# Kernel optimization log

Hardware: AMD Instinct MI355X
Metric: run time of the kernel (lower is better)

The kernel has to match this reference:

```python
import jax, jax.numpy as jnp
import numpy as np

K = 3
STRIDE = 1
PAD = 1


def _conv2d(x, w, b):
    y = jax.lax.conv_general_dilated(
        x, w, window_strides=(STRIDE, STRIDE),
        padding=[(PAD, PAD), (PAD, PAD)],
        dimension_numbers=("NCHW", "OIHW", "NCHW"))
    return y + b[None, :, None, None]


def _bilinear_sample(xb, py, px):
    # xb: [C, H, W]; py, px: [K2, Ho, Wo] float sample coords
    C, H, W = xb.shape
    y0 = jnp.floor(py)
    x0 = jnp.floor(px)
    ay = py - y0  # frac weights
    ax = px - x0
    out = jnp.zeros((C,) + py.shape, dtype=xb.dtype)
    corners = [
        (y0, x0, (1.0 - ay) * (1.0 - ax)),
        (y0, x0 + 1.0, (1.0 - ay) * ax),
        (y0 + 1.0, x0, ay * (1.0 - ax)),
        (y0 + 1.0, x0 + 1.0, ay * ax),
    ]
    for yc, xc, wgt in corners:
        valid = (yc >= 0) & (yc < H) & (xc >= 0) & (xc < W)
        yi = jnp.clip(yc, 0, H - 1).astype(jnp.int32)
        xi = jnp.clip(xc, 0, W - 1).astype(jnp.int32)
        g = xb[:, yi, xi]  # [C, K2, Ho, Wo]
        out = out + g * (wgt * valid.astype(xb.dtype))[None]
    return out


def _deform_forward(x, weight, bias, p_weight, p_bias):
    B, Cin, H, W = x.shape
    Cout = weight.shape[0]
    K2 = K * K
    # offset / mask prediction conv
    pout = _conv2d(x, p_weight, p_bias)  # [B, 3*K2, Ho, Wo]
    o1, o2, m = jnp.split(pout, 3, axis=1)
    offset = jnp.concatenate([o1, o2], axis=1)  # [B, 2*K2, Ho, Wo]
    mask = jax.nn.sigmoid(m)  # [B, K2, Ho, Wo]
    Ho, Wo = mask.shape[2], mask.shape[3]
    # torchvision layout: channel 2k = dy_k, 2k+1 = dx_k
    off = offset.reshape(B, K2, 2, Ho, Wo)
    dy, dx = off[:, :, 0], off[:, :, 1]  # [B, K2, Ho, Wo]
    ki = (jnp.arange(K2) // K).astype(x.dtype)  # kernel row
    kj = (jnp.arange(K2) % K).astype(x.dtype)   # kernel col
    base_y = jnp.arange(Ho, dtype=x.dtype) * STRIDE - PAD  # [Ho]
    base_x = jnp.arange(Wo, dtype=x.dtype) * STRIDE - PAD  # [Wo]
    py = base_y[None, None, :, None] + ki[None, :, None, None] + dy
    px = base_x[None, None, None, :] + kj[None, :, None, None] + dx
    sampled = jax.vmap(_bilinear_sample)(x, py, px)  # [B, Cin, K2, Ho, Wo]
    sampled = sampled * mask[:, None]
    w = weight.reshape(Cout, Cin, K2)
    out = jnp.einsum('bckhw,ock->bohw', sampled, w) + bias[None, :, None, None]
    return out


def setup_inputs() -> dict:
    key = jax.random.key(0)
    k1, k2, k3 = jax.random.split(key, 3)
    B, Cin, Cout, H, W = 4, 256, 256, 64, 64
    x = jax.random.normal(k1, (B, Cin, H, W), dtype=jnp.float32)
    fan_in = Cin * K * K
    weight = jax.random.normal(k2, (Cout, Cin, K, K), dtype=jnp.float32) / np.sqrt(fan_in)
    bias = jnp.zeros((Cout,), dtype=jnp.float32)
    # small random offset/mask predictor (zero-init in the original; randomized
    # here so the deformable sampling path is exercised)
    p_weight = jax.random.normal(k3, (3 * K * K, Cin, K, K), dtype=jnp.float32) * 0.02
    p_bias = jnp.zeros((3 * K * K,), dtype=jnp.float32)
    return {"x": x, "weight": weight, "bias": bias, "p_weight": p_weight, "p_bias": p_bias}


def reference(x, weight, bias, p_weight, p_bias):
    return _deform_forward(x, weight, bias, p_weight, p_bias)
```

## Files before the change

### kernel.cpp

```cpp
#include <hip/hip_runtime.h>
#include <stdint.h>


#define CIN 256
#define COUT 256
#define HWS 4096
#define MTOT 16384
#define KTOT 2304
#define SPLITK 8

typedef __attribute__((ext_vector_type(8))) short bf16x8;
typedef __attribute__((ext_vector_type(4))) float f32x4;

__device__ __forceinline__ unsigned short f2bf(float f) {
  unsigned int u = __float_as_uint(f);
  unsigned int r = (u + 0x7fffu + ((u >> 16) & 1u)) >> 16;
  return (unsigned short)r;
}
__device__ __forceinline__ float bf2f(unsigned short u) {
  return __uint_as_float(((unsigned int)u) << 16);
}

__device__ __forceinline__ void gload_lds16(const void* g, void* l) {
  __builtin_amdgcn_global_load_lds((const __attribute__((address_space(1))) void*)g,
                                   (__attribute__((address_space(3))) void*)l, 16, 0, 0);
}

__global__ __launch_bounds__(256) void prep_and_transpose(const float* __restrict__ x,
                                                          const float* __restrict__ w,
                                                          const float* __restrict__ pw,
                                                          unsigned short* __restrict__ xt,
                                                          unsigned short* __restrict__ WB,
                                                          unsigned short* __restrict__ PWs,
                                                          unsigned short* __restrict__ zerop) {
  __shared__ float tile[32][33];
  int bid = blockIdx.x;
  if (bid < 4096) {
    int b = bid >> 10;
    int rest = bid & 1023;
    int hw0 = (rest & 127) * 32;
    int c0 = ((rest >> 7) & 7) * 32;
    int tx = threadIdx.x & 31, ty = threadIdx.x >> 5;
    for (int i = ty; i < 32; i += 8)
      tile[i][tx] = x[(size_t)(b * CIN + c0 + i) * HWS + hw0 + tx];
    __syncthreads();
    for (int r = ty; r < 32; r += 8)
      xt[(size_t)(b * HWS + hw0 + r) * CIN + c0 + tx] = f2bf(tile[tx][r]);
  } else {
    int idx = (bid - 4096) * 256 + threadIdx.x;
    if (idx < 512)
      *(uint4*)(zerop + idx * 8) = make_uint4(0, 0, 0, 0);
    if (idx < KTOT * COUT) {
      int f = idx;
      int e = f & 7;
      int row = (f >> 3) & 15;
      int quad = (f >> 7) & 3;
      int j = (f >> 9) & 15;
      int t = f >> 13;
      int kk = t * 32 + quad * 8 + e;
      int o = j * 16 + row;
      int k = kk >> 8, c = kk & 255;
      WB[f] = f2bf(w[o * KTOT + c * 9 + k]);
    } else {
      int f2 = idx - KTOT * COUT;
      int t_ = f2 & 7;
      int rest = f2 >> 3;
      int j = rest & 31;
      int kk = (rest >> 5) * 8 + t_;
      int k = kk >> 8, c = kk & 255;
      float v = (j < 27) ? pw[j * KTOT + c * 9 + k] : 0.0f;
      PWs[f2] = f2bf(v);
    }
  }
}

__global__ __launch_bounds__(256) void offset_conv_sk(const unsigned short* __restrict__ xt,
                                                      const unsigned short* __restrict__ PWs,
                                                      const unsigned short* __restrict__ zerop,
                                                      float* __restrict__ Pbuf) {
  __shared__ unsigned short Al[64 * 32];
  __shared__ unsigned short Bl[1024];
  int tid = threadIdx.x;
  int lane = tid & 63, wv = tid >> 6;
  int mt = (blockIdx.x & 7) * 32 + (blockIdx.x >> 3);
  int m0 = mt * 64;
  int s = blockIdx.y;
  int b = m0 >> 12;
  int hw0 = m0 & 4095;
  f32x4 acc[2] = {};

  for (int tt = 0; tt < 72 / SPLITK; ++tt) {
    int t = s * (72 / SPLITK) + tt;
    int k = t >> 3, c0 = (t & 7) * 32;
    int dyk = k / 3 - 1;
    int dxk = k % 3 - 1;
    __syncthreads();
    if (tid < 128)
      gload_lds16(PWs + (size_t)t * 1024 + tid * 8, &Bl[tid * 8]);
    {
      int r = tid >> 2;
      int hw = hw0 + r;
      int h = hw >> 6, wwp = hw & 63;
      int y = h + dyk, xx = wwp + dxk;
      bool valid = ((unsigned)y < 64u) && ((unsigned)xx < 64u);
      const unsigned short* src = valid
          ? xt + ((size_t)((b << 12) + (y << 6) + xx) << 8) + c0 + (tid & 3) * 8
          : zerop;
      gload_lds16(src, &Al[tid * 8]);
    }
    __syncthreads();
    int row = lane & 15, quad = lane >> 4;
    bf16x8 af = *(const bf16x8*)&Al[(wv * 16 + row) * 32 + quad * 8];
    for (int j = 0; j < 2; ++j) {
      bf16x8 bfr = *(const bf16x8*)&Bl[(quad * 32 + j * 16 + row) * 8];
      acc[j] = __builtin_amdgcn_mfma_f32_16x16x32_bf16(af, bfr, acc[j], 0, 0, 0);
    }
  }

  int row = lane & 15, quad = lane >> 4;
  for (int j = 0; j < 2; ++j) {
    int n = j * 16 + row;
    for (int r_ = 0; r_ < 4; ++r_) {
      int m = m0 + wv * 16 + quad * 4 + r_;
      Pbuf[((size_t)s * MTOT + m) * 32 + n] = acc[j][r_];
    }
  }
}

__global__ __launch_bounds__(256) void sample9(const unsigned short* __restrict__ xt,
                                               const float* __restrict__ Pbuf,
                                               const float* __restrict__ p_bias,
                                               unsigned short* __restrict__ A) {
  __shared__ int4 dI[4][9];
  __shared__ float4 dW[4][9];
  int tid = threadIdx.x;
  int reg = blockIdx.x & 7;
  int mb = reg * 2048 + (blockIdx.x >> 3) * 4;

  if (tid < 36) {
    int lm = tid / 9, k = tid - lm * 9;
    int m = mb + lm;
    float dy = p_bias[2 * k];
    float dx = p_bias[2 * k + 1];
    float mv = p_bias[18 + k];
#pragma unroll
    for (int s = 0; s < SPLITK; ++s) {
      const float* p = Pbuf + ((size_t)s * MTOT + m) * 32;
      dy += p[2 * k];
      dx += p[2 * k + 1];
      mv += p[18 + k];
    }
    float mk = 1.0f / (1.0f + __expf(-mv));

    int hw = m & 4095, h = hw >> 6, ww = hw & 63;
    float py = (float)(h - 1 + k / 3) + dy;
    float px = (float)(ww - 1 + k % 3) + dx;
    float y0f = floorf(py), x0f = floorf(px);
    float ay = py - y0f, ax = px - x0f;
    int y0 = (int)y0f, x0 = (int)x0f;

    float w00 = (1.f - ay) * (1.f - ax) * mk;
    float w01 = (1.f - ay) * ax * mk;
    float w10 = ay * (1.f - ax) * mk;
    float w11 = ay * ax * mk;

    float vy0 = ((unsigned)y0 < 64u) ? 1.f : 0.f;
    float vy1 = ((unsigned)(y0 + 1) < 64u) ? 1.f : 0.f;
    float vx0 = ((unsigned)x0 < 64u) ? 1.f : 0.f;
    float vx1 = ((unsigned)(x0 + 1) < 64u) ? 1.f : 0.f;
    w00 *= vy0 * vx0; w01 *= vy0 * vx1; w10 *= vy1 * vx0; w11 *= vy1 * vx1;

    int yc0 = min(max(y0, 0), 63), yc1 = min(max(y0 + 1, 0), 63);
    int xc0 = min(max(x0, 0), 63), xc1 = min(max(x0 + 1, 0), 63);

    dI[lm][k] = make_int4((yc0 * 64 + xc0) * 256, (yc0 * 64 + xc1) * 256,
                          (yc1 * 64 + xc0) * 256, (yc1 * 64 + xc1) * 256);
    dW[lm][k] = make_float4(w00, w01, w10, w11);
  }
  __syncthreads();

  int wv = tid >> 6, lane = tid & 63;
  int m = mb + wv;
  int b = m >> 12;
  const unsigned short* xtb = xt + (((size_t)b << 12) << 8);
  unsigned short* abase = A + (((size_t)(m >> 4) * 72 + (lane >> 3)) * 16 + (m & 15)) * 32
                            + ((lane >> 1) & 3) * 8 + (lane & 1) * 4;

#pragma unroll
  for (int k = 0; k < 9; ++k) {
    int4 o4 = dI[wv][k];
    float4 w4 = dW[wv][k];
    ushort4 t00 = *(const ushort4*)(xtb + o4.x + 4 * lane);
    ushort4 t01 = *(const ushort4*)(xtb + o4.y + 4 * lane);
    ushort4 t10 = *(const ushort4*)(xtb + o4.z + 4 * lane);
    ushort4 t11 = *(const ushort4*)(xtb + o4.w + 4 * lane);
    float r0 = w4.x * bf2f(t00.x) + w4.y * bf2f(t01.x) + w4.z * bf2f(t10.x) + w4.w * bf2f(t11.x);
    float r1 = w4.x * bf2f(t00.y) + w4.y * bf2f(t01.y) + w4.z * bf2f(t10.y) + w4.w * bf2f(t11.y);
    float r2 = w4.x * bf2f(t00.z) + w4.y * bf2f(t01.z) + w4.z * bf2f(t10.z) + w4.w * bf2f(t11.z);
    float r3 = w4.x * bf2f(t00.w) + w4.y * bf2f(t01.w) + w4.z * bf2f(t10.w) + w4.w * bf2f(t11.w);
    ushort4 o;
    o.x = f2bf(r0); o.y = f2bf(r1); o.z = f2bf(r2); o.w = f2bf(r3);
    *(ushort4*)(abase + (size_t)k * 8 * 512) = o;
  }
}

__global__ __launch_bounds__(256) void main_gemm(const unsigned short* __restrict__ A2,
                                                 const unsigned short* __restrict__ WB,
                                                 const float* __restrict__ bias,
                                                 float* __restrict__ out) {
  int tid = threadIdx.x;
  int lane = tid & 63, wv = tid >> 6;
  int m0 = blockIdx.x * 128;
  int n0 = blockIdx.y * 64;
  int wm = wv * 32;
  int row = lane & 15, quad = lane >> 4;
  f32x4 acc[2][4] = {};

  int mb0 = (m0 + wm) >> 4;
  const unsigned short* aptr0 = A2 + (size_t)mb0 * 72 * 512 + row * 32 + quad * 8;
  const unsigned short* aptr1 = aptr0 + (size_t)72 * 512;
  const unsigned short* bptr = WB + (size_t)(blockIdx.y * 4) * 512 + quad * 128 + row * 8;

  bf16x8 a0c = *(const bf16x8*)(aptr0);
  bf16x8 a1c = *(const bf16x8*)(aptr1);
  bf16x8 bc0 = *(const bf16x8*)(bptr);
  bf16x8 bc1 = *(const bf16x8*)(bptr + 512);
  bf16x8 bc2 = *(const bf16x8*)(bptr + 1024);
  bf16x8 bc3 = *(const bf16x8*)(bptr + 1536);

  for (int t = 0; t < 72; ++t) {
    bf16x8 a0n, a1n, bn0, bn1, bn2, bn3;
    if (t < 71) {
      a0n = *(const bf16x8*)(aptr0 + (t + 1) * 512);
      a1n = *(const bf16x8*)(aptr1 + (t + 1) * 512);
      const unsigned short* bt = bptr + (size_t)(t + 1) * 8192;
      bn0 = *(const bf16x8*)(bt);
      bn1 = *(const bf16x8*)(bt + 512);
      bn2 = *(const bf16x8*)(bt + 1024);
      bn3 = *(const bf16x8*)(bt + 1536);
    }
    acc[0][0] = __builtin_amdgcn_mfma_f32_16x16x32_bf16(a0c, bc0, acc[0][0], 0, 0, 0);
    acc[0][1] = __builtin_amdgcn_mfma_f32_16x16x32_bf16(a0c, bc1, acc[0][1], 0, 0, 0);
    acc[0][2] = __builtin_amdgcn_mfma_f32_16x16x32_bf16(a0c, bc2, acc[0][2], 0, 0, 0);
    acc[0][3] = __builtin_amdgcn_mfma_f32_16x16x32_bf16(a0c, bc3, acc[0][3], 0, 0, 0);
    acc[1][0] = __builtin_amdgcn_mfma_f32_16x16x32_bf16(a1c, bc0, acc[1][0], 0, 0, 0);
    acc[1][1] = __builtin_amdgcn_mfma_f32_16x16x32_bf16(a1c, bc1, acc[1][1], 0, 0, 0);
    acc[1][2] = __builtin_amdgcn_mfma_f32_16x16x32_bf16(a1c, bc2, acc[1][2], 0, 0, 0);
    acc[1][3] = __builtin_amdgcn_mfma_f32_16x16x32_bf16(a1c, bc3, acc[1][3], 0, 0, 0);
    a0c = a0n; a1c = a1n;
    bc0 = bn0; bc1 = bn1; bc2 = bn2; bc3 = bn3;
  }

  int b = m0 >> 12, hw0 = m0 & 4095;
#pragma unroll
  for (int j = 0; j < 4; ++j) {
    int o = n0 + j * 16 + row;
    float bo = bias[o];
#pragma unroll
    for (int i = 0; i < 2; ++i) {
      int hw = hw0 + wm + i * 16 + quad * 4;
      float4 v;
      v.x = acc[i][j][0] + bo;
      v.y = acc[i][j][1] + bo;
      v.z = acc[i][j][2] + bo;
      v.w = acc[i][j][3] + bo;
      *(float4*)(out + (((size_t)(b * COUT + o)) << 12) + hw) = v;
    }
  }
}

extern "C" void kernel_launch(void* const* d_in, const int* in_sizes, int n_in,
                              void* d_out, int out_size, void* d_ws, size_t ws_size,
                              hipStream_t stream) {
  const float* x        = (const float*)d_in[0];
  const float* weight   = (const float*)d_in[1];
  const float* bias     = (const float*)d_in[2];
  const float* p_weight = (const float*)d_in[3];
  const float* p_bias   = (const float*)d_in[4];
  float* out = (float*)d_out;
  char* ws = (char*)d_ws;

  const size_t OFF_XT   = 0;
  const size_t OFF_WB   = OFF_XT + 8388608;
  const size_t OFF_PW   = OFF_WB + 1179648;
  const size_t OFF_P    = OFF_PW + 147456;
  const size_t OFF_ZP   = OFF_P + 16777216;
  const size_t OFF_A    = OFF_ZP + 8192;

  unsigned short* xt    = (unsigned short*)(ws + OFF_XT);
  unsigned short* WB    = (unsigned short*)(ws + OFF_WB);
  unsigned short* PWs   = (unsigned short*)(ws + OFF_PW);
  float* Pbuf           = (float*)(ws + OFF_P);
  unsigned short* zerop = (unsigned short*)(ws + OFF_ZP);
  unsigned short* Amat  = (unsigned short*)(ws + OFF_A);

  prep_and_transpose<<<4096 + 2592, 256, 0, stream>>>(x, weight, p_weight, xt, WB, PWs, zerop);
  offset_conv_sk<<<dim3(MTOT / 64, SPLITK), 256, 0, stream>>>(xt, PWs, zerop, Pbuf);
  sample9<<<MTOT / 4, 256, 0, stream>>>(xt, Pbuf, p_bias, Amat);
  main_gemm<<<dim3(MTOT / 128, COUT / 64), 256, 0, stream>>>(Amat, WB, bias, out);
}
```

Before: 150.3 us.

## Deepen main GEMM register prefetch to four stages and remap blocks per XCD

The main GEMM loop previously prefetched only one k-step ahead. It now keeps four register-staged sets of A/B fragments in flight, so global-load latency is better hidden behind MFMAs. The grid is flattened to 512 blocks and remapped so that the blocks on each XCD share A rows across the four N tiles, which should improve L2 reuse. The extra in-flight fragments raise VGPR pressure and could reduce occupancy.

```diff
diff --git a/kernel.cpp b/kernel.cpp
--- a/kernel.cpp
+++ b/kernel.cpp
@@ -204,52 +204,76 @@
   }
 }
 
+#define LOADSET(SA0, SA1, SB0, SB1, SB2, SB3, TT)                         \
+  {                                                                       \
+    const unsigned short* a0_ = ap0 + (size_t)(TT) * 512;                 \
+    const unsigned short* a1_ = ap1 + (size_t)(TT) * 512;                 \
+    const unsigned short* bt_ = bp + (size_t)(TT) * 8192;                 \
+    SA0 = *(const bf16x8*)(a0_);                                          \
+    SA1 = *(const bf16x8*)(a1_);                                          \
+    SB0 = *(const bf16x8*)(bt_);                                          \
+    SB1 = *(const bf16x8*)(bt_ + 512);                                    \
+    SB2 = *(const bf16x8*)(bt_ + 1024);                                   \
+    SB3 = *(const bf16x8*)(bt_ + 1536);                                   \
+  }
+
+#define COMPUTESET(SA0, SA1, SB0, SB1, SB2, SB3)                                        \
+  acc[0][0] = __builtin_amdgcn_mfma_f32_16x16x32_bf16(SA0, SB0, acc[0][0], 0, 0, 0);    \
+  acc[0][1] = __builtin_amdgcn_mfma_f32_16x16x32_bf16(SA0, SB1, acc[0][1], 0, 0, 0);    \
+  acc[0][2] = __builtin_amdgcn_mfma_f32_16x16x32_bf16(SA0, SB2, acc[0][2], 0, 0, 0);    \
+  acc[0][3] = __builtin_amdgcn_mfma_f32_16x16x32_bf16(SA0, SB3, acc[0][3], 0, 0, 0);    \
+  acc[1][0] = __builtin_amdgcn_mfma_f32_16x16x32_bf16(SA1, SB0, acc[1][0], 0, 0, 0);    \
+  acc[1][1] = __builtin_amdgcn_mfma_f32_16x16x32_bf16(SA1, SB1, acc[1][1], 0, 0, 0);    \
+  acc[1][2] = __builtin_amdgcn_mfma_f32_16x16x32_bf16(SA1, SB2, acc[1][2], 0, 0, 0);    \
+  acc[1][3] = __builtin_amdgcn_mfma_f32_16x16x32_bf16(SA1, SB3, acc[1][3], 0, 0, 0);
+
 __global__ __launch_bounds__(256) void main_gemm(const unsigned short* __restrict__ A2,
                                                  const unsigned short* __restrict__ WB,
                                                  const float* __restrict__ bias,
                                                  float* __restrict__ out) {
   int tid = threadIdx.x;
   int lane = tid & 63, wv = tid >> 6;
-  int m0 = blockIdx.x * 128;
-  int n0 = blockIdx.y * 64;
+  int bid = blockIdx.x;
+  int xcd = bid & 7;
+  int wgrp = bid >> 3;
+  int mt = xcd * 16 + (wgrp >> 2);
+  int nb = wgrp & 3;
+  int m0 = mt * 128;
+  int n0 = nb * 64;
   int wm = wv * 32;
   int row = lane & 15, quad = lane >> 4;
   f32x4 acc[2][4] = {};
 
   int mb0 = (m0 + wm) >> 4;
-  const unsigned short* aptr0 = A2 + (size_t)mb0 * 72 * 512 + row * 32 + quad * 8;
-  const unsigned short* aptr1 = aptr0 + (size_t)72 * 512;
-  const unsigned short* bptr = WB + (size_t)(blockIdx.y * 4) * 512 + quad * 128 + row * 8;
-
-  bf16x8 a0c = *(const bf16x8*)(aptr0);
-  bf16x8 a1c = *(const bf16x8*)(aptr1);
-  bf16x8 bc0 = *(const bf16x8*)(bptr);
-  bf16x8 bc1 = *(const bf16x8*)(bptr + 512);
-  bf16x8 bc2 = *(const bf16x8*)(bptr + 1024);
-  bf16x8 bc3 = *(const bf16x8*)(bptr + 1536);
-
-  for (int t = 0; t < 72; ++t) {
-    bf16x8 a0n, a1n, bn0, bn1, bn2, bn3;
-    if (t < 71) {
-      a0n = *(const bf16x8*)(aptr0 + (t + 1) * 512);
-      a1n = *(const bf16x8*)(aptr1 + (t + 1) * 512);
-      const unsigned short* bt = bptr + (size_t)(t + 1) * 8192;
-      bn0 = *(const bf16x8*)(bt);
-      bn1 = *(const bf16x8*)(bt + 512);
-      bn2 = *(const bf16x8*)(bt + 1024);
-      bn3 = *(const bf16x8*)(bt + 1536);
-    }
-    acc[0][0] = __builtin_amdgcn_mfma_f32_16x16x32_bf16(a0c, bc0, acc[0][0], 0, 0, 0);
-    acc[0][1] = __builtin_amdgcn_mfma_f32_16x16x32_bf16(a0c, bc1, acc[0][1], 0, 0, 0);
-    acc[0][2] = __builtin_amdgcn_mfma_f32_16x16x32_bf16(a0c, bc2, acc[0][2], 0, 0, 0);
-    acc[0][3] = __builtin_amdgcn_mfma_f32_16x16x32_bf16(a0c, bc3, acc[0][3], 0, 0, 0);
-    acc[1][0] = __builtin_amdgcn_mfma_f32_16x16x32_bf16(a1c, bc0, acc[1][0], 0, 0, 0);
-    acc[1][1] = __builtin_amdgcn_mfma_f32_16x16x32_bf16(a1c, bc1, acc[1][1], 0, 0, 0);
-    acc[1][2] = __builtin_amdgcn_mfma_f32_16x16x32_bf16(a1c, bc2, acc[1][2], 0, 0, 0);
-    acc[1][3] = __builtin_amdgcn_mfma_f32_16x16x32_bf16(a1c, bc3, acc[1][3], 0, 0, 0);
-    a0c = a0n; a1c = a1n;
-    bc0 = bn0; bc1 = bn1; bc2 = bn2; bc3 = bn3;
-  }
+  const unsigned short* ap0 = A2 + (size_t)mb0 * 72 * 512 + row * 32 + quad * 8;
+  const unsigned short* ap1 = ap0 + (size_t)72 * 512;
+  const unsigned short* bp = WB + (size_t)(nb * 4) * 512 + quad * 128 + row * 8;
+
+  bf16x8 s0a0, s0a1, s0b0, s0b1, s0b2, s0b3;
+  bf16x8 s1a0, s1a1, s1b0, s1b1, s1b2, s1b3;
+  bf16x8 s2a0, s2a1, s2b0, s2b1, s2b2, s2b3;
+  bf16x8 s3a0, s3a1, s3b0, s3b1, s3b2, s3b3;
+
+  LOADSET(s0a0, s0a1, s0b0, s0b1, s0b2, s0b3, 0)
+  LOADSET(s1a0, s1a1, s1b0, s1b1, s1b2, s1b3, 1)
+  LOADSET(s2a0, s2a1, s2b0, s2b1, s2b2, s2b3, 2)
+  LOADSET(s3a0, s3a1, s3b0, s3b1, s3b2, s3b3, 3)
+
+#pragma unroll 1
+  for (int t = 0; t < 68; t += 4) {
+    COMPUTESET(s0a0, s0a1, s0b0, s0b1, s0b2, s0b3)
+    LOADSET(s0a0, s0a1, s0b0, s0b1, s0b2, s0b3, t + 4)
+    COMPUTESET(s1a0, s1a1, s1b0, s1b1, s1b2, s1b3)
+    LOADSET(s1a0, s1a1, s1b0, s1b1, s1b2, s1b3, t + 5)
+    COMPUTESET(s2a0, s2a1, s2b0, s2b1, s2b2, s2b3)
+    LOADSET(s2a0, s2a1, s2b0, s2b1, s2b2, s2b3, t + 6)
+    COMPUTESET(s3a0, s3a1, s3b0, s3b1, s3b2, s3b3)
+    LOADSET(s3a0, s3a1, s3b0, s3b1, s3b2, s3b3, t + 7)
+  }
+  COMPUTESET(s0a0, s0a1, s0b0, s0b1, s0b2, s0b3)
+  COMPUTESET(s1a0, s1a1, s1b0, s1b1, s1b2, s1b3)
+  COMPUTESET(s2a0, s2a1, s2b0, s2b1, s2b2, s2b3)
+  COMPUTESET(s3a0, s3a1, s3b0, s3b1, s3b2, s3b3)
 
   int b = m0 >> 12, hw0 = m0 & 4095;
 #pragma unroll
@@ -297,5 +321,5 @@
   prep_and_transpose<<<4096 + 2592, 256, 0, stream>>>(x, weight, p_weight, xt, WB, PWs, zerop);
   offset_conv_sk<<<dim3(MTOT / 64, SPLITK), 256, 0, stream>>>(xt, PWs, zerop, Pbuf);
   sample9<<<MTOT / 4, 256, 0, stream>>>(xt, Pbuf, p_bias, Amat);
-  main_gemm<<<dim3(MTOT / 128, COUT / 64), 256, 0, stream>>>(Amat, WB, bias, out);
-}
+  main_gemm<<<512, 256, 0, stream>>>(Amat, WB, bias, out);
+}
```

Measured after the change: 148.2 us. About the same (-1.4%).
